# Performance work log

Measured on AMD Instinct MI355X. Metric: run time of the kernel, lower is better.

The kernel has to match this reference:

```python
import jax, jax.numpy as jnp
import numpy as np

OUT_FEATURES = 4096
IN_FEATURES = 4096
NUMEL = OUT_FEATURES * IN_FEATURES          # 16777216
NUM_SUPER = NUMEL // 256                    # 65536 superblocks of 256 weights


def setup_inputs() -> dict:
    key = jax.random.key(0)
    k_x, k_p, k_d, k_dm, k_s, k_m = jax.random.split(key, 6)
    x = jax.random.normal(k_x, (2, 2048, IN_FEATURES), dtype=jnp.float32)
    # packed bytes: two 4-bit quants per byte
    packed = jax.random.randint(k_p, (NUMEL // 2,), 0, 256, dtype=jnp.int32)
    # per-superblock fp scale/min (small positive values like real Q4_K 'd'/'dmin')
    d = jax.random.uniform(k_d, (NUM_SUPER,), dtype=jnp.float32) * 0.02
    dmin = jax.random.uniform(k_dm, (NUM_SUPER,), dtype=jnp.float32) * 0.02
    # per-subblock 6-bit scale/min quants (8 subblocks per superblock)
    scales = jax.random.randint(k_s, (NUM_SUPER * 8,), 0, 64, dtype=jnp.int32)
    mins = jax.random.randint(k_m, (NUM_SUPER * 8,), 0, 64, dtype=jnp.int32)
    return {"x": x, "packed": packed, "d": d, "dmin": dmin,
            "scales": scales, "mins": mins}


def _q4_k_dequantize(packed, d, dmin, scales, mins):
    # nibble split: low then high, interleaved per byte (stack dim=1 + flatten)
    low = packed & 15
    high = (packed >> 4) & 15
    q = jnp.stack([low, high], axis=1).reshape(-1).astype(jnp.float32)  # [NUMEL]
    blocks = q.reshape(NUM_SUPER, 8, 32)
    blk_scale = (scales.astype(jnp.float32) / 63.0).reshape(NUM_SUPER, 8, 1)
    blk_min = (mins.astype(jnp.float32) / 63.0).reshape(NUM_SUPER, 8, 1)
    normalized = blocks / 15.0 * blk_scale + blk_min
    w = normalized * d.reshape(NUM_SUPER, 1, 1) + dmin.reshape(NUM_SUPER, 1, 1)
    return w.reshape(OUT_FEATURES, IN_FEATURES)


def reference(x, packed, d, dmin, scales, mins):
    w = _q4_k_dequantize(packed, d, dmin, scales, mins).astype(x.dtype)
    # F.linear(x, w) = x @ w.T ; bias is None
    return jnp.einsum('bsk,nk->bsn', x, w)
```

## Files before the change

### kernel.cpp

```cpp
#include <hip/hip_runtime.h>
#include <stdint.h>

#define M_DIM 4096
#define K_DIM 4096
#define N_DIM 4096

typedef float f32x4 __attribute__((ext_vector_type(4)));
typedef int   i32x4 __attribute__((ext_vector_type(4)));

__global__ __launch_bounds__(256) void quant_xw(const float* __restrict__ x,
                                                const int* __restrict__ packed,
                                                const float* __restrict__ d,
                                                const float* __restrict__ dmin,
                                                const int* __restrict__ scales,
                                                const int* __restrict__ mins,
                                                int8_t* __restrict__ xq,
                                                float* __restrict__ sx,
                                                int8_t* __restrict__ wq,
                                                float* __restrict__ sw) {
    const int wave = threadIdx.x >> 6;
    const int lane = threadIdx.x & 63;
    if (blockIdx.x < 1024) {
        const int row = blockIdx.x * 4 + wave;
        const float4* xr = (const float4*)(x + (size_t)row * K_DIM);
        float4 v[16];
#pragma unroll
        for (int c = 0; c < 16; ++c) v[c] = xr[c * 64 + lane];
        float am = 0.f;
#pragma unroll
        for (int c = 0; c < 16; ++c) {
            am = fmaxf(am, fabsf(v[c].x)); am = fmaxf(am, fabsf(v[c].y));
            am = fmaxf(am, fabsf(v[c].z)); am = fmaxf(am, fabsf(v[c].w));
        }
#pragma unroll
        for (int off = 32; off; off >>= 1) am = fmaxf(am, __shfl_xor(am, off, 64));
        am = fmaxf(am, 1e-20f);
        const float inv = 127.0f / am;
        int* oq = (int*)(xq + (size_t)row * K_DIM);
#pragma unroll
        for (int c = 0; c < 16; ++c) {
            int q0 = __float2int_rn(v[c].x * inv);
            int q1 = __float2int_rn(v[c].y * inv);
            int q2 = __float2int_rn(v[c].z * inv);
            int q3 = __float2int_rn(v[c].w * inv);
            oq[c * 64 + lane] = (q0 & 255) | ((q1 & 255) << 8) |
                                ((q2 & 255) << 16) | ((q3 & 255) << 24);
        }
        if (lane == 0) sx[row] = am / 127.0f;
    } else {
        const int n = (blockIdx.x - 1024) * 4 + wave;
        const int sb = n * 128;
        const float s0  = (float)scales[sb + lane];
        const float s1  = (float)scales[sb + 64 + lane];
        const float mn0 = (float)mins[sb + lane];
        const float mn1 = (float)mins[sb + 64 + lane];
        const int di = n * 16;
        const float dd0 = d[di + (lane >> 3)];
        const float dd1 = d[di + 8 + (lane >> 3)];
        const float dm0 = dmin[di + (lane >> 3)];
        const float dm1 = dmin[di + 8 + (lane >> 3)];
        const float a0 = dd0 * s0 * (1.0f / 945.0f);
        const float b0 = dd0 * mn0 * (1.0f / 63.0f) + dm0;
        const float a1 = dd1 * s1 * (1.0f / 945.0f);
        const float b1 = dd1 * mn1 * (1.0f / 63.0f) + dm1;
        float m = fmaxf(15.0f * a0 + b0, 15.0f * a1 + b1);
#pragma unroll
        for (int off = 32; off; off >>= 1) m = fmaxf(m, __shfl_xor(m, off, 64));
        m = fmaxf(m, 1e-20f);
        const float inv = 127.0f / m;
        const float A0 = a0 * inv, B0 = b0 * inv;
        const float A1 = a1 * inv, B1 = b1 * inv;
        const int4* pr = (const int4*)(packed + (size_t)n * (K_DIM / 2));
        int2* outr = (int2*)(wq + (size_t)n * K_DIM);
#pragma unroll
        for (int c = 0; c < 8; ++c) {
            const int4 pv = pr[c * 64 + lane];
            const int sIdx = (c & 3) * 16 + (lane >> 2);
            const float a = (c < 4) ? __shfl(A0, sIdx, 64) : __shfl(A1, sIdx, 64);
            const float b = (c < 4) ? __shfl(B0, sIdx, 64) : __shfl(B1, sIdx, 64);
            int q0 = __float2int_rn((float)(pv.x & 15) * a + b);
            int q1 = __float2int_rn((float)((pv.x >> 4) & 15) * a + b);
            int q2 = __float2int_rn((float)(pv.y & 15) * a + b);
            int q3 = __float2int_rn((float)((pv.y >> 4) & 15) * a + b);
            int q4 = __float2int_rn((float)(pv.z & 15) * a + b);
            int q5 = __float2int_rn((float)((pv.z >> 4) & 15) * a + b);
            int q6 = __float2int_rn((float)(pv.w & 15) * a + b);
            int q7 = __float2int_rn((float)((pv.w >> 4) & 15) * a + b);
            int2 o;
            o.x = (q0 & 255) | ((q1 & 255) << 8) | ((q2 & 255) << 16) | ((q3 & 255) << 24);
            o.y = (q4 & 255) | ((q5 & 255) << 8) | ((q6 & 255) << 16) | ((q7 & 255) << 24);
            outr[c * 64 + lane] = o;
        }
        if (lane == 0) sw[n] = m / 127.0f;
    }
}

#define BK 128

__device__ __forceinline__ void async_copy16(void* lds, const void* g) {
    __builtin_amdgcn_global_load_lds(
        (const __attribute__((address_space(1))) void*)g,
        (__attribute__((address_space(3))) void*)lds, 16, 0, 0);
}

#define BARRIER() asm volatile("s_barrier" ::: "memory")
#define WAITV(n)  asm volatile("s_waitcnt vmcnt(" #n ")" ::: "memory")
#define LGKM0()   asm volatile("s_waitcnt lgkmcnt(0)" ::: "memory")
#define mfma64(a, b, c) __builtin_amdgcn_mfma_i32_16x16x64_i8(a, b, c, 0, 0, 0)

__global__ __launch_bounds__(512, 2) void gemm_i8(const int8_t* __restrict__ A,
                                                  const int8_t* __restrict__ B,
                                                  const float* __restrict__ sx,
                                                  const float* __restrict__ sw,
                                                  float* __restrict__ C) {
    __shared__ int8_t sA[2][2][128 * 128];
    __shared__ int8_t sB[2][2][128 * 128];

    const int tid  = threadIdx.x;
    const int wave = tid >> 6;
    const int lane = tid & 63;
    const int wm = wave >> 1;
    const int wn = wave & 1;
    const int r4 = lane & 15;
    const int q  = lane >> 4;
    const int ah = wm >> 1;

    const int bid = blockIdx.x;
    const int lid = (bid & 7) * 32 + (bid >> 3);
    const int m0 = (lid & 15) * 256;
    const int n0 = (lid >> 4) * 256;

    i32x4 acc[4][8] = {};
    i32x4 aF[2][4];
    i32x4 bFa[2][2], bFb[2][2];

    const int rowS = tid >> 3;
    const int cS   = (tid & 7) ^ (rowS & 7);
    const size_t rs64 = (size_t)64 * K_DIM;
    const int8_t* gAh[2];
    const int8_t* gBh[2];
    gAh[0] = A + (size_t)(m0 + rowS) * K_DIM + cS * 16;
    gAh[1] = gAh[0] + (size_t)128 * K_DIM;
    gBh[0] = B + (size_t)(n0 + rowS) * K_DIM + cS * 16;
    gBh[1] = gBh[0] + (size_t)128 * K_DIM;
    const int ldsW = wave * 1024;

#define STAGE_A(buf, half, koff)                                          \
    do {                                                                  \
        async_copy16(&sA[buf][half][ldsW],        gAh[half] + (koff));    \
        async_copy16(&sA[buf][half][ldsW + 8192], gAh[half] + rs64 + (koff)); \
    } while (0)
#define STAGE_B(buf, half, koff)                                          \
    do {                                                                  \
        async_copy16(&sB[buf][half][ldsW],        gBh[half] + (koff));    \
        async_copy16(&sB[buf][half][ldsW + 8192], gBh[half] + rs64 + (koff)); \
    } while (0)

    int aOffB[2], bOffB[2];
#pragma unroll
    for (int ks = 0; ks < 2; ++ks) {
        const int sl = (((ks * 4 + q) ^ (r4 & 7)) * 16);
        aOffB[ks] = ((wm & 1) * 64 + r4) * 128 + sl;
        bOffB[ks] = r4 * 128 + sl;
    }

#define RD_A(buf, ks, m) (*(const i32x4*)&sA[buf][ah][aOffB[ks] + (m) * 2048])
#define RD_B(buf, ks, n) (*(const i32x4*)&sB[buf][wn][bOffB[ks] + (n) * 2048])

#define MMA_BW(g, BC, BN, rb, ng)                                         \
    do {                                                                  \
        __builtin_amdgcn_s_setprio(1);                                    \
        _Pragma("unroll") for (int m = 0; m < 4; ++m)                     \
        _Pragma("unroll") for (int nn = 0; nn < 2; ++nn)                  \
            acc[m][2*(g)+nn] = mfma64(aF[0][m], BC[0][nn], acc[m][2*(g)+nn]); \
        BN[0][0] = RD_B(rb, 0, 2*(ng));                                  \
        BN[0][1] = RD_B(rb, 0, 2*(ng) + 1);                              \
        _Pragma("unroll") for (int m = 0; m < 4; ++m)                     \
        _Pragma("unroll") for (int nn = 0; nn < 2; ++nn)                  \
            acc[m][2*(g)+nn] = mfma64(aF[1][m], BC[1][nn], acc[m][2*(g)+nn]); \
        BN[1][0] = RD_B(rb, 1, 2*(ng));                                  \
        BN[1][1] = RD_B(rb, 1, 2*(ng) + 1);                              \
        __builtin_amdgcn_s_setprio(0);                                    \
    } while (0)

#define MMA_P4(BC, BN, nb)                                                \
    do {                                                                  \
        __builtin_amdgcn_s_setprio(1);                                    \
        _Pragma("unroll") for (int m = 0; m < 4; ++m)                     \
        _Pragma("unroll") for (int nn = 0; nn < 2; ++nn)                  \
            acc[m][6+nn] = mfma64(aF[0][m], BC[0][nn], acc[m][6+nn]);     \
        _Pragma("unroll") for (int m = 0; m < 4; ++m)                     \
            aF[0][m] = RD_A(nb, 0, m);                                    \
        BN[0][0] = RD_B(nb, 0, 0);                                        \
        BN[0][1] = RD_B(nb, 0, 1);                                        \
        _Pragma("unroll") for (int m = 0; m < 4; ++m)                     \
        _Pragma("unroll") for (int nn = 0; nn < 2; ++nn)                  \
            acc[m][6+nn] = mfma64(aF[1][m], BC[1][nn], acc[m][6+nn]);     \
        _Pragma("unroll") for (int m = 0; m < 4; ++m)                     \
            aF[1][m] = RD_A(nb, 1, m);                                    \
        BN[1][0] = RD_B(nb, 1, 0);                                        \
        BN[1][1] = RD_B(nb, 1, 1);                                        \
        __builtin_amdgcn_s_setprio(0);                                    \
    } while (0)

#define MMA_END(BC)                                                       \
    do {                                                                  \
        __builtin_amdgcn_s_setprio(1);                                    \
        _Pragma("unroll") for (int m = 0; m < 4; ++m)                     \
        _Pragma("unroll") for (int nn = 0; nn < 2; ++nn)                  \
            acc[m][6+nn] = mfma64(aF[0][m], BC[0][nn], acc[m][6+nn]);     \
        _Pragma("unroll") for (int m = 0; m < 4; ++m)                     \
        _Pragma("unroll") for (int nn = 0; nn < 2; ++nn)                  \
            acc[m][6+nn] = mfma64(aF[1][m], BC[1][nn], acc[m][6+nn]);     \
        __builtin_amdgcn_s_setprio(0);                                    \
    } while (0)

#define TILE(p, koA, koB)                                                 \
    do {                                                                  \
        STAGE_B((p)^1, 0, koB); STAGE_B((p)^1, 1, koB); STAGE_A(p, 0, koA); \
        MMA_BW(0, bFa, bFb, p, 1);                                        \
        STAGE_A(p, 1, koA);                                               \
        MMA_BW(1, bFb, bFa, p, 2);                                        \
        WAITV(2); BARRIER();                                              \
        MMA_BW(2, bFa, bFb, p, 3);                                        \
        MMA_P4(bFb, bFa, (p)^1);                                          \
        WAITV(2); BARRIER();                                              \
    } while (0)

    STAGE_A(0, 0, 0); STAGE_A(0, 1, 0); STAGE_B(0, 0, 0); STAGE_B(0, 1, 0);
    WAITV(0);
    BARRIER();
#pragma unroll
    for (int m = 0; m < 4; ++m) { aF[0][m] = RD_A(0, 0, m); aF[1][m] = RD_A(0, 1, m); }
#pragma unroll
    for (int nn = 0; nn < 2; ++nn) { bFa[0][nn] = RD_B(0, 0, nn); bFa[1][nn] = RD_B(0, 1, nn); }
    LGKM0();
    BARRIER();
    STAGE_A(1, 0, BK); STAGE_A(1, 1, BK);

#pragma unroll 1
    for (int i = 0; i < 15; ++i) {
        const int t2 = 2 * i;
        TILE(0, (t2 + 2) * BK, (t2 + 1) * BK);
        TILE(1, (t2 + 3) * BK, (t2 + 2) * BK);
    }

    STAGE_B(1, 0, 31 * BK); STAGE_B(1, 1, 31 * BK);
    MMA_BW(0, bFa, bFb, 0, 1);
    MMA_BW(1, bFb, bFa, 0, 2);
    WAITV(2); BARRIER();
    MMA_BW(2, bFa, bFb, 0, 3);
    MMA_P4(bFb, bFa, 1);
    WAITV(0); BARRIER();
    MMA_BW(0, bFa, bFb, 1, 1);
    MMA_BW(1, bFb, bFa, 1, 2);
    MMA_BW(2, bFa, bFb, 1, 3);
    MMA_END(bFb);

#pragma unroll
    for (int m = 0; m < 4; ++m) {
        const int rbase = m0 + wm * 64 + m * 16 + q * 4;
        const float4 s4 = *(const float4*)&sx[rbase];
#pragma unroll
        for (int n = 0; n < 8; ++n) {
            const int col = n0 + wn * 128 + n * 16 + r4;
            const float swc = sw[col];
            float* cp = C + (size_t)rbase * N_DIM + col;
            cp[0 * N_DIM] = (float)acc[m][n][0] * s4.x * swc;
            cp[1 * N_DIM] = (float)acc[m][n][1] * s4.y * swc;
            cp[2 * N_DIM] = (float)acc[m][n][2] * s4.z * swc;
            cp[3 * N_DIM] = (float)acc[m][n][3] * s4.w * swc;
        }
    }
#undef STAGE_A
#undef STAGE_B
#undef RD_A
#undef RD_B
#undef MMA_BW
#undef MMA_P4
#undef MMA_END
#undef TILE
}

extern "C" void kernel_launch(void* const* d_in, const int* in_sizes, int n_in,
                              void* d_out, int out_size, void* d_ws, size_t ws_size,
                              hipStream_t stream) {
    const float* x      = (const float*)d_in[0];
    const int*   packed = (const int*)d_in[1];
    const float* d      = (const float*)d_in[2];
    const float* dmin   = (const float*)d_in[3];
    const int*   scales = (const int*)d_in[4];
    const int*   mins   = (const int*)d_in[5];
    float* out = (float*)d_out;

    int8_t* xq = (int8_t*)d_ws;
    int8_t* wq = xq + (size_t)M_DIM * K_DIM;
    float*  sx = (float*)(wq + (size_t)N_DIM * K_DIM);
    float*  sw = sx + M_DIM;

    quant_xw<<<2048, 256, 0, stream>>>(x, packed, d, dmin, scales, mins,
                                       xq, sx, wq, sw);
    gemm_i8<<<256, 512, 0, stream>>>(xq, wq, sx, sw, out);
}
```

Measured before the change: 220.1 us.

## Shrink int8 GEMM tile to 128x128 with 4 waves and 1024 blocks

Replaces the 256x256 block tile (8 waves, 256 blocks) with a 128x128 tile using 4 waves and 1024 blocks, and rewrites the staging and MFMA pipeline to match. Each wave still computes a 64x64 sub-tile, but LDS per block drops to 64KB and more blocks become available. This aims at better occupancy and load balance across the 256 CUs, since the old grid gave only one block per CU. The cost is more global/L2 traffic, because each block now reuses its A and B tiles over half as many outputs.

```diff
diff --git a/kernel.cpp b/kernel.cpp
--- a/kernel.cpp
+++ b/kernel.cpp
@@ -108,13 +108,13 @@
 #define LGKM0()   asm volatile("s_waitcnt lgkmcnt(0)" ::: "memory")
 #define mfma64(a, b, c) __builtin_amdgcn_mfma_i32_16x16x64_i8(a, b, c, 0, 0, 0)
 
-__global__ __launch_bounds__(512, 2) void gemm_i8(const int8_t* __restrict__ A,
+__global__ __launch_bounds__(256, 2) void gemm_i8(const int8_t* __restrict__ A,
                                                   const int8_t* __restrict__ B,
                                                   const float* __restrict__ sx,
                                                   const float* __restrict__ sw,
                                                   float* __restrict__ C) {
-    __shared__ int8_t sA[2][2][128 * 128];
-    __shared__ int8_t sB[2][2][128 * 128];
+    __shared__ int8_t sA[2][128 * 128];
+    __shared__ int8_t sB[2][128 * 128];
 
     const int tid  = threadIdx.x;
     const int wave = tid >> 6;
@@ -123,147 +123,137 @@
     const int wn = wave & 1;
     const int r4 = lane & 15;
     const int q  = lane >> 4;
-    const int ah = wm >> 1;
 
     const int bid = blockIdx.x;
-    const int lid = (bid & 7) * 32 + (bid >> 3);
-    const int m0 = (lid & 15) * 256;
-    const int n0 = (lid >> 4) * 256;
-
-    i32x4 acc[4][8] = {};
+    const int lid = (bid & 7) * 128 + (bid >> 3);
+    const int m0 = (lid & 31) * 128;
+    const int n0 = (lid >> 5) * 128;
+
+    i32x4 acc[4][4] = {};
     i32x4 aF[2][4];
     i32x4 bFa[2][2], bFb[2][2];
 
     const int rowS = tid >> 3;
     const int cS   = (tid & 7) ^ (rowS & 7);
-    const size_t rs64 = (size_t)64 * K_DIM;
-    const int8_t* gAh[2];
-    const int8_t* gBh[2];
-    gAh[0] = A + (size_t)(m0 + rowS) * K_DIM + cS * 16;
-    gAh[1] = gAh[0] + (size_t)128 * K_DIM;
-    gBh[0] = B + (size_t)(n0 + rowS) * K_DIM + cS * 16;
-    gBh[1] = gBh[0] + (size_t)128 * K_DIM;
+    const size_t rs32 = (size_t)32 * K_DIM;
+    const int8_t* gA = A + (size_t)(m0 + rowS) * K_DIM + cS * 16;
+    const int8_t* gB = B + (size_t)(n0 + rowS) * K_DIM + cS * 16;
     const int ldsW = wave * 1024;
 
-#define STAGE_A(buf, half, koff)                                          \
-    do {                                                                  \
-        async_copy16(&sA[buf][half][ldsW],        gAh[half] + (koff));    \
-        async_copy16(&sA[buf][half][ldsW + 8192], gAh[half] + rs64 + (koff)); \
-    } while (0)
-#define STAGE_B(buf, half, koff)                                          \
-    do {                                                                  \
-        async_copy16(&sB[buf][half][ldsW],        gBh[half] + (koff));    \
-        async_copy16(&sB[buf][half][ldsW + 8192], gBh[half] + rs64 + (koff)); \
+#define STAGE_A(buf, koff)                                                \
+    do {                                                                  \
+        async_copy16(&sA[buf][ldsW],         gA + (koff));                \
+        async_copy16(&sA[buf][4096 + ldsW],  gA + rs32 + (koff));         \
+        async_copy16(&sA[buf][8192 + ldsW],  gA + 2 * rs32 + (koff));     \
+        async_copy16(&sA[buf][12288 + ldsW], gA + 3 * rs32 + (koff));     \
+    } while (0)
+#define STAGE_B(buf, koff)                                                \
+    do {                                                                  \
+        async_copy16(&sB[buf][ldsW],         gB + (koff));                \
+        async_copy16(&sB[buf][4096 + ldsW],  gB + rs32 + (koff));         \
+        async_copy16(&sB[buf][8192 + ldsW],  gB + 2 * rs32 + (koff));     \
+        async_copy16(&sB[buf][12288 + ldsW], gB + 3 * rs32 + (koff));     \
     } while (0)
 
     int aOffB[2], bOffB[2];
 #pragma unroll
     for (int ks = 0; ks < 2; ++ks) {
         const int sl = (((ks * 4 + q) ^ (r4 & 7)) * 16);
-        aOffB[ks] = ((wm & 1) * 64 + r4) * 128 + sl;
-        bOffB[ks] = r4 * 128 + sl;
-    }
-
-#define RD_A(buf, ks, m) (*(const i32x4*)&sA[buf][ah][aOffB[ks] + (m) * 2048])
-#define RD_B(buf, ks, n) (*(const i32x4*)&sB[buf][wn][bOffB[ks] + (n) * 2048])
-
-#define MMA_BW(g, BC, BN, rb, ng)                                         \
-    do {                                                                  \
-        __builtin_amdgcn_s_setprio(1);                                    \
-        _Pragma("unroll") for (int m = 0; m < 4; ++m)                     \
-        _Pragma("unroll") for (int nn = 0; nn < 2; ++nn)                  \
-            acc[m][2*(g)+nn] = mfma64(aF[0][m], BC[0][nn], acc[m][2*(g)+nn]); \
-        BN[0][0] = RD_B(rb, 0, 2*(ng));                                  \
-        BN[0][1] = RD_B(rb, 0, 2*(ng) + 1);                              \
-        _Pragma("unroll") for (int m = 0; m < 4; ++m)                     \
-        _Pragma("unroll") for (int nn = 0; nn < 2; ++nn)                  \
-            acc[m][2*(g)+nn] = mfma64(aF[1][m], BC[1][nn], acc[m][2*(g)+nn]); \
-        BN[1][0] = RD_B(rb, 1, 2*(ng));                                  \
-        BN[1][1] = RD_B(rb, 1, 2*(ng) + 1);                              \
-        __builtin_amdgcn_s_setprio(0);                                    \
-    } while (0)
-
-#define MMA_P4(BC, BN, nb)                                                \
-    do {                                                                  \
-        __builtin_amdgcn_s_setprio(1);                                    \
-        _Pragma("unroll") for (int m = 0; m < 4; ++m)                     \
-        _Pragma("unroll") for (int nn = 0; nn < 2; ++nn)                  \
-            acc[m][6+nn] = mfma64(aF[0][m], BC[0][nn], acc[m][6+nn]);     \
-        _Pragma("unroll") for (int m = 0; m < 4; ++m)                     \
-            aF[0][m] = RD_A(nb, 0, m);                                    \
-        BN[0][0] = RD_B(nb, 0, 0);                                        \
-        BN[0][1] = RD_B(nb, 0, 1);                                        \
-        _Pragma("unroll") for (int m = 0; m < 4; ++m)                     \
-        _Pragma("unroll") for (int nn = 0; nn < 2; ++nn)                  \
-            acc[m][6+nn] = mfma64(aF[1][m], BC[1][nn], acc[m][6+nn]);     \
-        _Pragma("unroll") for (int m = 0; m < 4; ++m)                     \
-            aF[1][m] = RD_A(nb, 1, m);                                    \
-        BN[1][0] = RD_B(nb, 1, 0);                                        \
-        BN[1][1] = RD_B(nb, 1, 1);                                        \
-        __builtin_amdgcn_s_setprio(0);                                    \
-    } while (0)
-
-#define MMA_END(BC)                                                       \
-    do {                                                                  \
-        __builtin_amdgcn_s_setprio(1);                                    \
-        _Pragma("unroll") for (int m = 0; m < 4; ++m)                     \
-        _Pragma("unroll") for (int nn = 0; nn < 2; ++nn)                  \
-            acc[m][6+nn] = mfma64(aF[0][m], BC[0][nn], acc[m][6+nn]);     \
-        _Pragma("unroll") for (int m = 0; m < 4; ++m)                     \
-        _Pragma("unroll") for (int nn = 0; nn < 2; ++nn)                  \
-            acc[m][6+nn] = mfma64(aF[1][m], BC[1][nn], acc[m][6+nn]);     \
-        __builtin_amdgcn_s_setprio(0);                                    \
-    } while (0)
-
-#define TILE(p, koA, koB)                                                 \
-    do {                                                                  \
-        STAGE_B((p)^1, 0, koB); STAGE_B((p)^1, 1, koB); STAGE_A(p, 0, koA); \
-        MMA_BW(0, bFa, bFb, p, 1);                                        \
-        STAGE_A(p, 1, koA);                                               \
-        MMA_BW(1, bFb, bFa, p, 2);                                        \
-        WAITV(2); BARRIER();                                              \
-        MMA_BW(2, bFa, bFb, p, 3);                                        \
-        MMA_P4(bFb, bFa, (p)^1);                                          \
-        WAITV(2); BARRIER();                                              \
-    } while (0)
-
-    STAGE_A(0, 0, 0); STAGE_A(0, 1, 0); STAGE_B(0, 0, 0); STAGE_B(0, 1, 0);
-    WAITV(0);
+        aOffB[ks] = (wm * 64 + r4) * 128 + sl;
+        bOffB[ks] = (wn * 64 + r4) * 128 + sl;
+    }
+
+#define RD_A(buf, ks, m) (*(const i32x4*)&sA[buf][aOffB[ks] + (m) * 2048])
+#define RD_B(buf, ks, n) (*(const i32x4*)&sB[buf][bOffB[ks] + (n) * 2048])
+
+#define MMA_R1(p)                                                         \
+    do {                                                                  \
+        _Pragma("unroll") for (int m = 0; m < 4; ++m)                     \
+        _Pragma("unroll") for (int nn = 0; nn < 2; ++nn)                  \
+            acc[m][nn] = mfma64(aF[0][m], bFa[0][nn], acc[m][nn]);        \
+        bFb[0][0] = RD_B(p, 0, 2);                                        \
+        bFb[0][1] = RD_B(p, 0, 3);                                        \
+        _Pragma("unroll") for (int m = 0; m < 4; ++m)                     \
+        _Pragma("unroll") for (int nn = 0; nn < 2; ++nn)                  \
+            acc[m][nn] = mfma64(aF[1][m], bFa[1][nn], acc[m][nn]);        \
+        bFb[1][0] = RD_B(p, 1, 2);                                        \
+        bFb[1][1] = RD_B(p, 1, 3);                                        \
+    } while (0)
+
+#define MMA_R2(np)                                                        \
+    do {                                                                  \
+        _Pragma("unroll") for (int m = 0; m < 4; ++m)                     \
+        _Pragma("unroll") for (int nn = 0; nn < 2; ++nn)                  \
+            acc[m][2+nn] = mfma64(aF[0][m], bFb[0][nn], acc[m][2+nn]);    \
+        _Pragma("unroll") for (int m = 0; m < 4; ++m)                     \
+            aF[0][m] = RD_A(np, 0, m);                                    \
+        bFa[0][0] = RD_B(np, 0, 0);                                       \
+        bFa[0][1] = RD_B(np, 0, 1);                                       \
+        _Pragma("unroll") for (int m = 0; m < 4; ++m)                     \
+        _Pragma("unroll") for (int nn = 0; nn < 2; ++nn)                  \
+            acc[m][2+nn] = mfma64(aF[1][m], bFb[1][nn], acc[m][2+nn]);    \
+        _Pragma("unroll") for (int m = 0; m < 4; ++m)                     \
+            aF[1][m] = RD_A(np, 1, m);                                    \
+        bFa[1][0] = RD_B(np, 1, 0);                                       \
+        bFa[1][1] = RD_B(np, 1, 1);                                       \
+    } while (0)
+
+#define MMA_R2_END()                                                      \
+    do {                                                                  \
+        _Pragma("unroll") for (int m = 0; m < 4; ++m)                     \
+        _Pragma("unroll") for (int nn = 0; nn < 2; ++nn)                  \
+            acc[m][2+nn] = mfma64(aF[0][m], bFb[0][nn], acc[m][2+nn]);    \
+        _Pragma("unroll") for (int m = 0; m < 4; ++m)                     \
+        _Pragma("unroll") for (int nn = 0; nn < 2; ++nn)                  \
+            acc[m][2+nn] = mfma64(aF[1][m], bFb[1][nn], acc[m][2+nn]);    \
+    } while (0)
+
+#define TILE(p, koB, koA)                                                 \
+    do {                                                                  \
+        STAGE_B((p) ^ 1, koB);                                            \
+        STAGE_A(p, koA);                                                  \
+        MMA_R1(p);                                                        \
+        WAITV(4); BARRIER();                                              \
+        MMA_R2((p) ^ 1);                                                  \
+        BARRIER();                                                        \
+    } while (0)
+
+    STAGE_A(0, 0);
+    STAGE_B(0, 0);
+    STAGE_A(1, BK);
+    WAITV(4);
     BARRIER();
 #pragma unroll
-    for (int m = 0; m < 4; ++m) { aF[0][m] = RD_A(0, 0, m); aF[1][m] = RD_A(0, 1, m); }
-#pragma unroll
-    for (int nn = 0; nn < 2; ++nn) { bFa[0][nn] = RD_B(0, 0, nn); bFa[1][nn] = RD_B(0, 1, nn); }
+    for (int ks = 0; ks < 2; ++ks) {
+#pragma unroll
+        for (int m = 0; m < 4; ++m) aF[ks][m] = RD_A(0, ks, m);
+        bFa[ks][0] = RD_B(0, ks, 0);
+        bFa[ks][1] = RD_B(0, ks, 1);
+    }
     LGKM0();
     BARRIER();
-    STAGE_A(1, 0, BK); STAGE_A(1, 1, BK);
 
 #pragma unroll 1
     for (int i = 0; i < 15; ++i) {
-        const int t2 = 2 * i;
-        TILE(0, (t2 + 2) * BK, (t2 + 1) * BK);
-        TILE(1, (t2 + 3) * BK, (t2 + 2) * BK);
-    }
-
-    STAGE_B(1, 0, 31 * BK); STAGE_B(1, 1, 31 * BK);
-    MMA_BW(0, bFa, bFb, 0, 1);
-    MMA_BW(1, bFb, bFa, 0, 2);
-    WAITV(2); BARRIER();
-    MMA_BW(2, bFa, bFb, 0, 3);
-    MMA_P4(bFb, bFa, 1);
+        TILE(0, (2 * i + 1) * BK, (2 * i + 2) * BK);
+        TILE(1, (2 * i + 2) * BK, (2 * i + 3) * BK);
+    }
+
+    STAGE_B(1, 31 * BK);
+    MMA_R1(0);
     WAITV(0); BARRIER();
-    MMA_BW(0, bFa, bFb, 1, 1);
-    MMA_BW(1, bFb, bFa, 1, 2);
-    MMA_BW(2, bFa, bFb, 1, 3);
-    MMA_END(bFb);
+    MMA_R2(1);
+    BARRIER();
+    MMA_R1(1);
+    MMA_R2_END();
 
 #pragma unroll
     for (int m = 0; m < 4; ++m) {
         const int rbase = m0 + wm * 64 + m * 16 + q * 4;
         const float4 s4 = *(const float4*)&sx[rbase];
 #pragma unroll
-        for (int n = 0; n < 8; ++n) {
-            const int col = n0 + wn * 128 + n * 16 + r4;
+        for (int n = 0; n < 4; ++n) {
+            const int col = n0 + wn * 64 + n * 16 + r4;
             const float swc = sw[col];
             float* cp = C + (size_t)rbase * N_DIM + col;
             cp[0 * N_DIM] = (float)acc[m][n][0] * s4.x * swc;
@@ -276,9 +266,9 @@
 #undef STAGE_B
 #undef RD_A
 #undef RD_B
-#undef MMA_BW
-#undef MMA_P4
-#undef MMA_END
+#undef MMA_R1
+#undef MMA_R2
+#undef MMA_R2_END
 #undef TILE
 }
 
@@ -300,5 +290,5 @@
 
     quant_xw<<<2048, 256, 0, stream>>>(x, packed, d, dmin, scales, mins,
                                        xq, sx, wq, sw);
-    gemm_i8<<<256, 512, 0, stream>>>(xq, wq, sx, sw, out);
-}
+    gemm_i8<<<1024, 256, 0, stream>>>(xq, wq, sx, sw, out);
+}
```

Measured after the change: 224.4 us. No clear change (+2.0%).
